# Optimization experiments

Hardware: AMD Instinct MI355X
Metric: run time of the kernel (lower is better)

The kernel has to match this reference:

```python
import jax, jax.numpy as jnp
import numpy as np

EPS = 1e-12
B, C, H, M, E, P = 2, 20000, 64, 8, 200000, 3


def setup_inputs() -> dict:
    key = jax.random.key(0)
    ks = jax.random.split(key, 24)
    inp = {}
    inp["features"] = jax.random.normal(ks[0], (B, C, H), jnp.float32)
    inp["positions"] = jax.random.normal(ks[1], (B, C, P), jnp.float32)
    inp["edge_index"] = jax.random.randint(ks[2], (2, E), 0, C)
    inp["degree"] = jax.random.randint(ks[3], (C,), 1, 33).astype(jnp.float32)
    inp["cell_node_indices"] = jax.random.randint(ks[4], (C, M), 0, C)
    mask = (jax.random.uniform(ks[5], (C, M)) > 0.3).astype(jnp.float32)
    inp["cell_node_mask"] = mask.at[:, 0].set(1.0)  # first node always valid (pad semantics)

    def lin(k, fan_in, fan_out):
        return (jax.random.normal(k, (fan_in, fan_out), jnp.float32) / np.sqrt(fan_in)).astype(jnp.float32)

    # message MLP: Linear(2H+4 -> H), SiLU, Linear(H -> H)
    inp["W1"] = lin(ks[6], 2 * H + 4, H); inp["b1"] = jnp.zeros((H,), jnp.float32)
    inp["W2"] = lin(ks[7], H, H);         inp["b2"] = jnp.zeros((H,), jnp.float32)
    # position MLP: Linear(H -> H), SiLU, Linear(H -> 1)
    inp["P1"] = lin(ks[8], H, H);  inp["pb1"] = jnp.zeros((H,), jnp.float32)
    inp["P2"] = lin(ks[9], H, 1);  inp["pb2"] = jnp.zeros((1,), jnp.float32)
    # update MLP: Linear(2H -> H), SiLU, Linear(H -> H)
    inp["U1"] = lin(ks[10], 2 * H, H); inp["ub1"] = jnp.zeros((H,), jnp.float32)
    inp["U2"] = lin(ks[11], H, H);     inp["ub2"] = jnp.zeros((H,), jnp.float32)
    return inp


def _mlp(x, Wa, ba, Wb, bb):
    return jax.nn.silu(x @ Wa + ba) @ Wb + bb


def _forward(features, positions, edge_index, degree, cell_node_indices, cell_node_mask,
             W1, b1, W2, b2, P1, pb1, P2, pb2, U1, ub1, U2, ub2):
    src, dst = edge_index[0], edge_index[1]
    # gather padded node positions per cell: [B, C, M, P]
    node_pos = positions[:, cell_node_indices]

    h_src = features[:, src]                      # [B,E,H]
    h_dst = features[:, dst]
    rel = positions[:, src] - positions[:, dst]   # [B,E,P]
    dist = jnp.linalg.norm(rel, axis=-1, keepdims=True)  # [B,E,1]

    sp = node_pos[:, src]                         # [B,E,M,P]
    dp = node_pos[:, dst]
    mx = cell_node_mask[src]                      # [E,M]
    my = cell_node_mask[dst]

    # pairwise distances [B,E,M,M] via gram trick (avoids [B,E,M,M,P] intermediate)
    sp2 = jnp.sum(sp * sp, -1)                    # [B,E,M]
    dp2 = jnp.sum(dp * dp, -1)
    cross = jnp.einsum('bemp,benp->bemn', sp, dp)
    d = jnp.sqrt(jnp.maximum(sp2[..., :, None] + dp2[..., None, :] - 2.0 * cross, 0.0) + EPS)

    # masked pairwise-distance sum
    w = mx[:, :, None] * my[:, None, :]           # [E,M,M]
    pairwise = jnp.sum(d * w[None], axis=(-1, -2))  # [B,E]

    # centroid distance
    denx = jnp.maximum(mx.sum(-1, keepdims=True), EPS)  # [E,1]
    deny = jnp.maximum(my.sum(-1, keepdims=True), EPS)
    cx = jnp.sum(sp * mx[None, :, :, None], axis=2) / denx[None]  # [B,E,P]
    cy = jnp.sum(dp * my[None, :, :, None], axis=2) / deny[None]
    centroid = jnp.linalg.norm(cx - cy, axis=-1)  # [B,E]

    # Hausdorff distance (masked min/max)
    inf = jnp.float32(jnp.inf)
    d_xy = jnp.where(my[None, :, None, :] <= 0, inf, d)
    min_xy = jnp.where(mx[None] <= 0, 0.0, d_xy.min(-1))  # [B,E,M]
    h_xy = min_xy.max(-1)                                  # [B,E]
    d_yx = jnp.where(mx[None, :, None, :] <= 0, inf, jnp.swapaxes(d, -1, -2))
    min_yx = jnp.where(my[None] <= 0, 0.0, d_yx.min(-1))
    h_yx = min_yx.max(-1)
    haus = jnp.maximum(h_xy, h_yx)

    invariants = jnp.concatenate([dist, pairwise[..., None], centroid[..., None], haus[..., None]], -1)  # [B,E,4]
    msg_in = jnp.concatenate([h_src, h_dst, invariants], -1)  # [B,E,2H+4]
    messages = _mlp(msg_in, W1, b1, W2, b2)                   # [B,E,H]

    # scatter-aggregate into destination cells, degree-normalize
    agg = jnp.zeros_like(features).at[:, dst].add(messages)
    agg = agg / jnp.maximum(degree, 1.0)[None, :, None]

    # position update
    wts = jnp.tanh(_mlp(messages, P1, pb1, P2, pb2))          # [B,E,1]
    pos_upd = jnp.zeros_like(positions).at[:, dst].add(wts * rel)

    new_features = features + _mlp(jnp.concatenate([features, agg], -1), U1, ub1, U2, ub2)
    new_positions = positions + pos_upd
    return new_features, new_positions


def reference(features, positions, edge_index, degree, cell_node_indices, cell_node_mask,
              W1, b1, W2, b2, P1, pb1, P2, pb2, U1, ub1, U2, ub2):
    return _forward(features, positions, edge_index, degree, cell_node_indices, cell_node_mask,
                    W1, b1, W2, b2, P1, pb1, P2, pb2, U1, ub1, U2, ub2)
```

## Files before the change

kernel.cpp:

```cpp
#include <hip/hip_runtime.h>
#include <hip/hip_bf16.h>

#define B_ 2
#define C_ 20000
#define H_ 64
#define M_ 8
#define E_ 200000
#define P_ 3
#define EPS_ 1e-12f
#define ET_ (E_ / 64)

typedef __attribute__((ext_vector_type(8))) short short8;
typedef __attribute__((ext_vector_type(4))) float float4v;

__device__ __forceinline__ float silu_(float x) {
    return x / (1.f + __expf(-x));
}
__device__ __forceinline__ unsigned short f2b(float f) {
    unsigned u = __float_as_uint(f);
    unsigned r = (u + 0x7FFF + ((u >> 16) & 1)) >> 16;
    return (unsigned short)r;
}
__device__ __forceinline__ float b2f(unsigned short h) {
    return __uint_as_float(((unsigned)h) << 16);
}
__device__ __forceinline__ unsigned pk2u(float a, float b) {
    __hip_bfloat162 h = __float22bfloat162_rn(make_float2(a, b));
    unsigned u; __builtin_memcpy(&u, &h, sizeof(u)); return u;
}

#define W1S_OFF 0
#define W2S_OFF 8192
#define P1S_OFF 12288
#define U1S_OFF 16384
#define U2S_OFF 24576
#define WBUF_ELEMS 28672

#define NB_PREP  120
#define NB_FEATB 2500
#define NB_DESC  157
#define NB_HIST  782
#define NB_COMBO (NB_PREP + NB_FEATB + NB_DESC + NB_HIST)

__global__ __launch_bounds__(256) void combo_kernel(
    const float* __restrict__ W1, const float* __restrict__ W2,
    const float* __restrict__ P1, const float* __restrict__ U1,
    const float* __restrict__ U2, unsigned short* __restrict__ wbuf,
    const float* __restrict__ feat, unsigned short* __restrict__ featb,
    const float* __restrict__ pos, const int* __restrict__ cni,
    const float* __restrict__ mask, float* __restrict__ desc,
    const int* __restrict__ ei, int* __restrict__ cnt)
{
    const int bid = blockIdx.x;
    if (bid < NB_PREP) {
        int t = bid * 256 + threadIdx.x;
        if (t >= WBUF_ELEMS) return;
        const float* W; int e;
        if (t < W2S_OFF)      { W = W1; e = t; }
        else if (t < U1S_OFF) { W = (t < P1S_OFF) ? W2 : P1; e = (t < P1S_OFF) ? t - W2S_OFF : t - P1S_OFF; }
        else if (t < U2S_OFF) { W = U1; e = t - U1S_OFF; }
        else                  { W = U2; e = t - U2S_OFF; }
        int j = e & 7, lane = (e >> 3) & 63, nt = (e >> 9) & 3, kk = e >> 11;
        int k = kk * 32 + ((lane >> 4) * 8) + j;
        int n = nt * 16 + (lane & 15);
        wbuf[t] = f2b(W[k * 64 + n]);
    } else if (bid < NB_PREP + NB_FEATB) {
        int t = (bid - NB_PREP) * 256 + threadIdx.x;
        float4 v = *(const float4*)&feat[(size_t)t * 4];
        *(uint2*)&featb[(size_t)t * 4] = make_uint2(pk2u(v.x, v.y), pk2u(v.z, v.w));
    } else if (bid < NB_PREP + NB_FEATB + NB_DESC) {
        int tid = (bid - NB_PREP - NB_FEATB) * 256 + threadIdx.x;
        if (tid >= B_ * C_) return;
        int b = tid / C_, c = tid - b * C_;
        const float* pb = pos + (size_t)b * C_ * P_;
        float4* D = (float4*)(desc + (size_t)tid * 40);
        int4 n0 = *(const int4*)&cni[c*8];
        int4 n1 = *(const int4*)&cni[c*8 + 4];
        float4 m0 = *(const float4*)&mask[c*8];
        float4 m1 = *(const float4*)&mask[c*8 + 4];
        int ni[8] = {n0.x, n0.y, n0.z, n0.w, n1.x, n1.y, n1.z, n1.w};
        float mm[8] = {m0.x, m0.y, m0.z, m0.w, m1.x, m1.y, m1.z, m1.w};
        float sx = 0.f, sy = 0.f, sz = 0.f, sm = 0.f;
        #pragma unroll
        for (int m = 0; m < 8; ++m) {
            float x = pb[ni[m]*3+0], y = pb[ni[m]*3+1], z = pb[ni[m]*3+2];
            D[m] = make_float4(x, y, z, mm[m]);
            sx += x * mm[m]; sy += y * mm[m]; sz += z * mm[m]; sm += mm[m];
        }
        float inv = 1.f / fmaxf(sm, EPS_);
        D[8] = make_float4(sx * inv, sy * inv, sz * inv, sm);
        D[9] = make_float4(pb[c*3+0], pb[c*3+1], pb[c*3+2], 0.f);
    } else {
        int e = (bid - NB_PREP - NB_FEATB - NB_DESC) * 256 + threadIdx.x;
        if (e >= E_) return;
        atomicAdd(&cnt[ei[E_ + e]], 1);
    }
}

__global__ __launch_bounds__(256) void alloc_kernel(
    const int* __restrict__ cnt, int* __restrict__ cursor, int* __restrict__ total)
{
    int idx = blockIdx.x * 256 + threadIdx.x;
    int lane = threadIdx.x & 63;
    int v = (idx < C_) ? cnt[idx] : 0;
    int inc = v;
    #pragma unroll
    for (int s = 1; s < 64; s <<= 1) {
        int n = __shfl_up(inc, s);
        if (lane >= s) inc += n;
    }
    int wtot = __shfl(inc, 63);
    int base = 0;
    if (lane == 0) base = atomicAdd(total, wtot);
    base = __shfl(base, 0);
    if (idx < C_) cursor[idx] = base + inc - v;
}

__global__ __launch_bounds__(256) void scatter_kernel(
    const int* __restrict__ ei, int* __restrict__ cursor,
    int* __restrict__ ssrc, int* __restrict__ sdst)
{
    int e = blockIdx.x * 256 + threadIdx.x;
    if (e >= E_) return;
    int s = ei[e], d = ei[E_ + e];
    int slot = atomicAdd(&cursor[d], 1);
    ssrc[slot] = s;
    sdst[slot] = d;
}

__global__ __launch_bounds__(256) void edge_kernel(
    const unsigned short* __restrict__ featb,
    const int* __restrict__ ssrc, const int* __restrict__ sdst,
    const float* __restrict__ desc,
    const unsigned short* __restrict__ wbuf, const float* __restrict__ W1,
    const float* __restrict__ b1, const float* __restrict__ b2,
    const float* __restrict__ pb1, const float* __restrict__ P2,
    const float* __restrict__ pb2,
    float* __restrict__ aggf, float* __restrict__ out_pos)
{
    __shared__ unsigned short lds[4 * 3328];

    const int tid  = threadIdx.x;
    const int w    = tid >> 6;
    const int lane = tid & 63;
    const int q    = lane >> 4;
    const int l16  = lane & 15;
    const int w16  = w * 16;

    const int tile = blockIdx.x;
    const int b    = tile / ET_;
    const int i0   = (tile - b * ET_) * 64;
    const int s_l  = ssrc[i0 + lane];
    const int d_l  = sdst[i0 + lane];
    const unsigned short* fb = featb + (size_t)b * C_ * H_;

    unsigned short* Xw = lds + w * 3328;
    unsigned short* Hw = Xw + 2176;
    unsigned short* Mw = Xw;

    const int sg = __shfl(s_l, w16 + l16);
    const int dg = __shfl(d_l, w16 + l16);
    const float4* Ds = (const float4*)(desc + ((size_t)b * C_ + sg) * 40);
    const float4* Dd = (const float4*)(desc + ((size_t)b * C_ + dg) * 40);

    float4 S[8];
    float sp2[8], rowmin[8];
    const float INFV = __builtin_inff();
    #pragma unroll
    for (int i = 0; i < 8; ++i) {
        S[i] = Ds[i];
        sp2[i] = S[i].x*S[i].x + S[i].y*S[i].y + S[i].z*S[i].z;
        rowmin[i] = INFV;
    }
    float pair = 0.f, hyx = 0.f;
    #pragma unroll
    for (int jj = 0; jj < 2; ++jj) {
        float4 Dj = Dd[q*2 + jj];
        float dp2 = Dj.x*Dj.x + Dj.y*Dj.y + Dj.z*Dj.z;
        float colmin = INFV;
        #pragma unroll
        for (int i = 0; i < 8; ++i) {
            float cr = S[i].x*Dj.x + S[i].y*Dj.y + S[i].z*Dj.z;
            float dd = sqrtf(fmaxf(sp2[i] + dp2 - 2.f*cr, 0.f) + EPS_);
            pair += dd * S[i].w * Dj.w;
            rowmin[i] = (Dj.w  > 0.f) ? fminf(rowmin[i], dd) : rowmin[i];
            colmin    = (S[i].w > 0.f) ? fminf(colmin, dd)    : colmin;
        }
        hyx = fmaxf(hyx, (Dj.w > 0.f) ? colmin : 0.f);
    }
    pair += __shfl_xor(pair, 16);  pair += __shfl_xor(pair, 32);
    hyx = fmaxf(hyx, __shfl_xor(hyx, 16));  hyx = fmaxf(hyx, __shfl_xor(hyx, 32));
    #pragma unroll
    for (int i = 0; i < 8; ++i) {
        rowmin[i] = fminf(rowmin[i], __shfl_xor(rowmin[i], 16));
        rowmin[i] = fminf(rowmin[i], __shfl_xor(rowmin[i], 32));
    }
    float hxy = 0.f;
    #pragma unroll
    for (int i = 0; i < 8; ++i)
        hxy = fmaxf(hxy, (S[i].w > 0.f) ? rowmin[i] : 0.f);
    float4 Sc = Ds[8], Dc = Dd[8];
    float cdx = Sc.x - Dc.x, cdy = Sc.y - Dc.y, cdz = Sc.z - Dc.z;
    float4 Sp = Ds[9], Dp = Dd[9];
    const float relx = Sp.x - Dp.x, rely = Sp.y - Dp.y, relz = Sp.z - Dp.z;
    const float ivx = sqrtf(relx*relx + rely*rely + relz*relz);
    const float ivy = pair;
    const float ivz = sqrtf(cdx*cdx + cdy*cdy + cdz*cdz);
    const float ivw = fmaxf(hxy, hyx);

    const int rr4 = lane >> 4, c4 = lane & 15;
    #pragma unroll
    for (int it = 0; it < 4; ++it) {
        int rloc = it * 4 + rr4;
        int r = w16 + rloc;
        int sr = __shfl(s_l, r);
        int dr = __shfl(d_l, r);
        uint2 vs = *(const uint2*)&fb[(size_t)sr * 64 + c4 * 4];
        uint2 vd = *(const uint2*)&fb[(size_t)dr * 64 + c4 * 4];
        *(uint2*)&Xw[rloc*136 + c4*4]      = vs;
        *(uint2*)&Xw[rloc*136 + 64 + c4*4] = vd;
    }

    float4v acc[4];
    #pragma unroll
    for (int nt = 0; nt < 4; ++nt) {
        float bv = b1[nt*16 + l16];
        acc[nt] = (float4v){bv, bv, bv, bv};
    }
    #pragma unroll
    for (int kk = 0; kk < 4; ++kk) {
        short8 a = *(const short8*)&Xw[l16*136 + kk*32 + q*8];
        #pragma unroll
        for (int nt = 0; nt < 4; ++nt) {
            short8 bf = *(const short8*)&wbuf[W1S_OFF + (((kk*4 + nt)*64) + lane) * 8];
            acc[nt] = __builtin_amdgcn_mfma_f32_16x16x32_bf16(a, bf, acc[nt], 0, 0, 0);
        }
    }
    float4 iv[4];
    #pragma unroll
    for (int i = 0; i < 4; ++i) {
        int r = q*4 + i;
        iv[i] = make_float4(__shfl(ivx, r), __shfl(ivy, r),
                            __shfl(ivz, r), __shfl(ivw, r));
    }
    #pragma unroll
    for (int nt = 0; nt < 4; ++nt) {
        float wa = W1[128*64 + nt*16 + l16];
        float wb = W1[129*64 + nt*16 + l16];
        float wc = W1[130*64 + nt*16 + l16];
        float wd = W1[131*64 + nt*16 + l16];
        #pragma unroll
        for (int i = 0; i < 4; ++i)
            acc[nt][i] += iv[i].x*wa + iv[i].y*wb + iv[i].z*wc + iv[i].w*wd;
    }
    #pragma unroll
    for (int nt = 0; nt < 4; ++nt)
        #pragma unroll
        for (int i = 0; i < 4; ++i)
            Hw[(q*4 + i)*72 + nt*16 + l16] = f2b(silu_(acc[nt][i]));

    float4v mac[4];
    #pragma unroll
    for (int nt = 0; nt < 4; ++nt) {
        float bv = b2[nt*16 + l16];
        mac[nt] = (float4v){bv, bv, bv, bv};
    }
    #pragma unroll
    for (int kk = 0; kk < 2; ++kk) {
        short8 a = *(const short8*)&Hw[l16*72 + kk*32 + q*8];
        #pragma unroll
        for (int nt = 0; nt < 4; ++nt) {
            short8 bf = *(const short8*)&wbuf[W2S_OFF + (((kk*4 + nt)*64) + lane) * 8];
            mac[nt] = __builtin_amdgcn_mfma_f32_16x16x32_bf16(a, bf, mac[nt], 0, 0, 0);
        }
    }
    #pragma unroll
    for (int nt = 0; nt < 4; ++nt)
        #pragma unroll
        for (int i = 0; i < 4; ++i)
            Mw[(q*4 + i)*72 + nt*16 + l16] = f2b(mac[nt][i]);

    float4v gac[4];
    #pragma unroll
    for (int nt = 0; nt < 4; ++nt) {
        float bv = pb1[nt*16 + l16];
        gac[nt] = (float4v){bv, bv, bv, bv};
    }
    #pragma unroll
    for (int kk = 0; kk < 2; ++kk) {
        short8 a = *(const short8*)&Mw[l16*72 + kk*32 + q*8];
        #pragma unroll
        for (int nt = 0; nt < 4; ++nt) {
            short8 bf = *(const short8*)&wbuf[P1S_OFF + (((kk*4 + nt)*64) + lane) * 8];
            gac[nt] = __builtin_amdgcn_mfma_f32_16x16x32_bf16(a, bf, gac[nt], 0, 0, 0);
        }
    }
    float p2v[4];
    #pragma unroll
    for (int nt = 0; nt < 4; ++nt) p2v[nt] = P2[nt*16 + l16];
    const float pb2v = pb2[0];

    #pragma unroll
    for (int i = 0; i < 4; ++i) {
        float p = 0.f;
        #pragma unroll
        for (int nt = 0; nt < 4; ++nt) p += silu_(gac[nt][i]) * p2v[nt];
        p += __shfl_xor(p, 8);
        p += __shfl_xor(p, 4);
        p += __shfl_xor(p, 2);
        p += __shfl_xor(p, 1);
        float wt = tanhf(p + pb2v);
        if (l16 == 0) *(float*)&Mw[(q*4 + i)*72 + 64] = wt;
    }

    float mrow[16];
    #pragma unroll
    for (int rr = 0; rr < 16; ++rr) mrow[rr] = b2f(Mw[rr*72 + lane]);
    float wtl = *(const float*)&Mw[l16*72 + 64];

    float* aggB = aggf + (size_t)b * C_ * 64;
    float* opB  = out_pos + (size_t)b * C_ * 3;

    int dprev = __shfl(d_l, w16);
    float colacc = 0.f, pxa = 0.f, pya = 0.f, pza = 0.f;
    #pragma unroll
    for (int rr = 0; rr < 16; ++rr) {
        int dcur = __shfl(d_l, w16 + rr);
        if (dcur != dprev) {
            atomicAdd(&aggB[(size_t)dprev * 64 + lane], colacc);
            if (lane < 3) {
                float v = (lane == 0) ? pxa : (lane == 1) ? pya : pza;
                atomicAdd(&opB[(size_t)dprev * 3 + lane], v);
            }
            colacc = 0.f; pxa = 0.f; pya = 0.f; pza = 0.f;
            dprev = dcur;
        }
        float wt = __shfl(wtl, rr);
        colacc += mrow[rr];
        pxa += wt * __shfl(relx, rr);
        pya += wt * __shfl(rely, rr);
        pza += wt * __shfl(relz, rr);
    }
    atomicAdd(&aggB[(size_t)dprev * 64 + lane], colacc);
    if (lane < 3) {
        float v = (lane == 0) ? pxa : (lane == 1) ? pya : pza;
        atomicAdd(&opB[(size_t)dprev * 3 + lane], v);
    }
}

__global__ __launch_bounds__(256) void node_kernel(
    const float* __restrict__ feat, const unsigned short* __restrict__ featb,
    const float* __restrict__ aggf, const float* __restrict__ deg,
    const unsigned short* __restrict__ wbuf,
    const float* __restrict__ ub1, const float* __restrict__ ub2,
    float* __restrict__ out_feat)
{
    __shared__ unsigned short lds[4 * 3328];

    const int tid  = threadIdx.x;
    const int w    = tid >> 6;
    const int lane = tid & 63;
    const int q    = lane >> 4;
    const int l16  = lane & 15;
    const int g0   = blockIdx.x * 64;

    unsigned short* Xw = lds + w * 3328;
    unsigned short* Hw = Xw + 2176;

    const int rr4 = lane >> 4, c4 = lane & 15;
    #pragma unroll
    for (int it = 0; it < 4; ++it) {
        int rloc = it * 4 + rr4;
        int g = g0 + w*16 + rloc;
        int gc = (g >= C_) ? g - C_ : g;
        float sc = 1.f / fmaxf(deg[gc], 1.f);
        uint2  vf = *(const uint2*)&featb[(size_t)g * 64 + c4 * 4];
        float4 va = *(const float4*)&aggf[(size_t)g * 64 + c4 * 4];
        *(uint2*)&Xw[rloc*136 + c4*4]      = vf;
        *(uint2*)&Xw[rloc*136 + 64 + c4*4] =
            make_uint2(pk2u(va.x*sc, va.y*sc), pk2u(va.z*sc, va.w*sc));
    }

    float4v acc[4];
    #pragma unroll
    for (int nt = 0; nt < 4; ++nt) {
        float bv = ub1[nt*16 + l16];
        acc[nt] = (float4v){bv, bv, bv, bv};
    }
    #pragma unroll
    for (int kk = 0; kk < 4; ++kk) {
        short8 a = *(const short8*)&Xw[l16*136 + kk*32 + q*8];
        #pragma unroll
        for (int nt = 0; nt < 4; ++nt) {
            short8 bf = *(const short8*)&wbuf[U1S_OFF + (((kk*4 + nt)*64) + lane) * 8];
            acc[nt] = __builtin_amdgcn_mfma_f32_16x16x32_bf16(a, bf, acc[nt], 0, 0, 0);
        }
    }
    #pragma unroll
    for (int nt = 0; nt < 4; ++nt)
        #pragma unroll
        for (int i = 0; i < 4; ++i)
            Hw[(q*4 + i)*72 + nt*16 + l16] = f2b(silu_(acc[nt][i]));

    float4v oac[4];
    #pragma unroll
    for (int nt = 0; nt < 4; ++nt) {
        float bv = ub2[nt*16 + l16];
        oac[nt] = (float4v){bv, bv, bv, bv};
    }
    #pragma unroll
    for (int kk = 0; kk < 2; ++kk) {
        short8 a = *(const short8*)&Hw[l16*72 + kk*32 + q*8];
        #pragma unroll
        for (int nt = 0; nt < 4; ++nt) {
            short8 bf = *(const short8*)&wbuf[U2S_OFF + (((kk*4 + nt)*64) + lane) * 8];
            oac[nt] = __builtin_amdgcn_mfma_f32_16x16x32_bf16(a, bf, oac[nt], 0, 0, 0);
        }
    }
    #pragma unroll
    for (int nt = 0; nt < 4; ++nt)
        #pragma unroll
        for (int i = 0; i < 4; ++i) {
            size_t idx = (size_t)(g0 + w*16 + q*4 + i) * 64 + nt*16 + l16;
            out_feat[idx] = feat[idx] + oac[nt][i];
        }
}

extern "C" void kernel_launch(void* const* d_in, const int* in_sizes, int n_in,
                              void* d_out, int out_size, void* d_ws, size_t ws_size,
                              hipStream_t stream) {
    const float* feat = (const float*)d_in[0];
    const float* pos  = (const float*)d_in[1];
    const int*   ei   = (const int*)d_in[2];
    const float* deg  = (const float*)d_in[3];
    const int*   cni  = (const int*)d_in[4];
    const float* mask = (const float*)d_in[5];
    const float* W1   = (const float*)d_in[6];
    const float* b1   = (const float*)d_in[7];
    const float* W2   = (const float*)d_in[8];
    const float* b2   = (const float*)d_in[9];
    const float* P1   = (const float*)d_in[10];
    const float* pb1  = (const float*)d_in[11];
    const float* P2   = (const float*)d_in[12];
    const float* pb2  = (const float*)d_in[13];
    const float* U1   = (const float*)d_in[14];
    const float* ub1  = (const float*)d_in[15];
    const float* U2   = (const float*)d_in[16];
    const float* ub2  = (const float*)d_in[17];

    float* out_feat = (float*)d_out;
    float* out_pos  = out_feat + (size_t)B_ * C_ * H_;

    float* desc = (float*)d_ws;
    float* aggf = desc + (size_t)B_ * C_ * 40;
    unsigned short* featb = (unsigned short*)(aggf + (size_t)B_ * C_ * 64);
    unsigned short* wbuf  = featb + (size_t)B_ * C_ * 64;
    int* cnt    = (int*)(wbuf + WBUF_ELEMS);
    int* total  = cnt + C_;
    int* cursor = total + 1;
    int* ssrc   = cursor + C_;
    int* sdst   = ssrc + E_;

    hipMemsetAsync(cnt, 0, (C_ + 1) * sizeof(int), stream);
    hipMemsetAsync(aggf, 0, (size_t)B_ * C_ * 64 * sizeof(float), stream);
    hipMemcpyAsync(out_pos, pos, (size_t)B_ * C_ * P_ * sizeof(float),
                   hipMemcpyDeviceToDevice, stream);

    combo_kernel<<<NB_COMBO, 256, 0, stream>>>(
        W1, W2, P1, U1, U2, wbuf, feat, featb, pos, cni, mask, desc, ei, cnt);

    alloc_kernel<<<(C_ + 255) / 256, 256, 0, stream>>>(cnt, cursor, total);
    scatter_kernel<<<(E_ + 255) / 256, 256, 0, stream>>>(ei, cursor, ssrc, sdst);

    edge_kernel<<<B_ * ET_, 256, 0, stream>>>(
        featb, ssrc, sdst, desc, wbuf, W1, b1, b2, pb1, P2, pb2, aggf, out_pos);

    node_kernel<<<(B_ * C_) / 64, 256, 0, stream>>>(
        feat, featb, aggf, deg, wbuf, ub1, ub2, out_feat);
}
```

Before: 226.5 us.

## Fold aggregate zeroing and position copy into combo kernel; streamline edge math

Moves the aggf memset and the out_pos device copy into extra blocks of the combo kernel, removing two separate stream operations. The Hausdorff and pairwise distance loop now uses additive infinity masks and a fused per-column sum, which replaces the selects and multiplies. The position scatter is rewritten so that 48 lanes each issue one atomic per edge component, instead of a serial shuffle-accumulate with run-length flushing. Occupancy hints are added to the edge and node kernels. Per-edge position atomics raise the atomic count, and the launch-bound hint may cause register spills.

Result: slower. 252.0 us (+11.2%).

```diff
diff --git a/kernel.cpp b/kernel.cpp
--- a/kernel.cpp
+++ b/kernel.cpp
@@ -36,11 +36,13 @@
 #define U2S_OFF 24576
 #define WBUF_ELEMS 28672
 
-#define NB_PREP  120
-#define NB_FEATB 2500
-#define NB_DESC  157
-#define NB_HIST  782
-#define NB_COMBO (NB_PREP + NB_FEATB + NB_DESC + NB_HIST)
+#define NB_PREP   120
+#define NB_FEATB  2500
+#define NB_DESC   157
+#define NB_HIST   782
+#define NB_AGGZ   2500
+#define NB_PCPY   118
+#define NB_COMBO  (NB_PREP + NB_FEATB + NB_DESC + NB_HIST + NB_AGGZ + NB_PCPY)
 
 __global__ __launch_bounds__(256) void combo_kernel(
     const float* __restrict__ W1, const float* __restrict__ W2,
@@ -49,7 +51,8 @@
     const float* __restrict__ feat, unsigned short* __restrict__ featb,
     const float* __restrict__ pos, const int* __restrict__ cni,
     const float* __restrict__ mask, float* __restrict__ desc,
-    const int* __restrict__ ei, int* __restrict__ cnt)
+    const int* __restrict__ ei, int* __restrict__ cnt,
+    float* __restrict__ aggf, float* __restrict__ out_pos)
 {
     const int bid = blockIdx.x;
     if (bid < NB_PREP) {
@@ -90,10 +93,17 @@
         float inv = 1.f / fmaxf(sm, EPS_);
         D[8] = make_float4(sx * inv, sy * inv, sz * inv, sm);
         D[9] = make_float4(pb[c*3+0], pb[c*3+1], pb[c*3+2], 0.f);
-    } else {
+    } else if (bid < NB_PREP + NB_FEATB + NB_DESC + NB_HIST) {
         int e = (bid - NB_PREP - NB_FEATB - NB_DESC) * 256 + threadIdx.x;
         if (e >= E_) return;
         atomicAdd(&cnt[ei[E_ + e]], 1);
+    } else if (bid < NB_PREP + NB_FEATB + NB_DESC + NB_HIST + NB_AGGZ) {
+        int t = (bid - NB_PREP - NB_FEATB - NB_DESC - NB_HIST) * 256 + threadIdx.x;
+        ((float4*)aggf)[t] = make_float4(0.f, 0.f, 0.f, 0.f);
+    } else {
+        int t = (bid - NB_PREP - NB_FEATB - NB_DESC - NB_HIST - NB_AGGZ) * 256 + threadIdx.x;
+        if (t < (B_ * C_ * P_) / 4)
+            ((float4*)out_pos)[t] = ((const float4*)pos)[t];
     }
 }
 
@@ -128,7 +138,7 @@
     sdst[slot] = d;
 }
 
-__global__ __launch_bounds__(256) void edge_kernel(
+__global__ __launch_bounds__(256, 4) void edge_kernel(
     const unsigned short* __restrict__ featb,
     const int* __restrict__ ssrc, const int* __restrict__ sdst,
     const float* __restrict__ desc,
@@ -163,13 +173,14 @@
     const float4* Ds = (const float4*)(desc + ((size_t)b * C_ + sg) * 40);
     const float4* Dd = (const float4*)(desc + ((size_t)b * C_ + dg) * 40);
 
+    const float INFV = __builtin_inff();
     float4 S[8];
-    float sp2[8], rowmin[8];
-    const float INFV = __builtin_inff();
+    float a_i[8], infm_i[8], rowmin[8];
     #pragma unroll
     for (int i = 0; i < 8; ++i) {
         S[i] = Ds[i];
-        sp2[i] = S[i].x*S[i].x + S[i].y*S[i].y + S[i].z*S[i].z;
+        a_i[i] = S[i].x*S[i].x + S[i].y*S[i].y + S[i].z*S[i].z + EPS_;
+        infm_i[i] = (S[i].w > 0.f) ? 0.f : INFV;
         rowmin[i] = INFV;
     }
     float pair = 0.f, hyx = 0.f;
@@ -177,15 +188,18 @@
     for (int jj = 0; jj < 2; ++jj) {
         float4 Dj = Dd[q*2 + jj];
         float dp2 = Dj.x*Dj.x + Dj.y*Dj.y + Dj.z*Dj.z;
-        float colmin = INFV;
+        float infm_j = (Dj.w > 0.f) ? 0.f : INFV;
+        float colmin = INFV, psum = 0.f;
         #pragma unroll
         for (int i = 0; i < 8; ++i) {
             float cr = S[i].x*Dj.x + S[i].y*Dj.y + S[i].z*Dj.z;
-            float dd = sqrtf(fmaxf(sp2[i] + dp2 - 2.f*cr, 0.f) + EPS_);
-            pair += dd * S[i].w * Dj.w;
-            rowmin[i] = (Dj.w  > 0.f) ? fminf(rowmin[i], dd) : rowmin[i];
-            colmin    = (S[i].w > 0.f) ? fminf(colmin, dd)    : colmin;
-        }
+            float t  = (a_i[i] + dp2) - 2.f*cr;
+            float dd = sqrtf(fmaxf(t, EPS_));
+            psum = fmaf(dd, S[i].w, psum);
+            rowmin[i] = fminf(rowmin[i], dd + infm_j);
+            colmin    = fminf(colmin,    dd + infm_i[i]);
+        }
+        pair = fmaf(Dj.w, psum, pair);
         hyx = fmaxf(hyx, (Dj.w > 0.f) ? colmin : 0.f);
     }
     pair += __shfl_xor(pair, 16);  pair += __shfl_xor(pair, 32);
@@ -313,42 +327,40 @@
         if (l16 == 0) *(float*)&Mw[(q*4 + i)*72 + 64] = wt;
     }
 
-    float mrow[16];
-    #pragma unroll
-    for (int rr = 0; rr < 16; ++rr) mrow[rr] = b2f(Mw[rr*72 + lane]);
-    float wtl = *(const float*)&Mw[l16*72 + 64];
-
     float* aggB = aggf + (size_t)b * C_ * 64;
     float* opB  = out_pos + (size_t)b * C_ * 3;
 
+    float wtl = *(const float*)&Mw[l16*72 + 64];
+    float gx = wtl * relx, gy = wtl * rely, gz = wtl * relz;
+    int e3 = lane / 3;
+    int c3 = lane - e3 * 3;
+    float sx = __shfl(gx, e3);
+    float sy = __shfl(gy, e3);
+    float sz = __shfl(gz, e3);
+    float val = (c3 == 0) ? sx : (c3 == 1) ? sy : sz;
+    int de = __shfl(d_l, w16 + e3);
+    if (lane < 48) atomicAdd(&opB[(size_t)de * 3 + c3], val);
+
+    float mrow[16];
+    #pragma unroll
+    for (int rr = 0; rr < 16; ++rr) mrow[rr] = b2f(Mw[rr*72 + lane]);
+
     int dprev = __shfl(d_l, w16);
-    float colacc = 0.f, pxa = 0.f, pya = 0.f, pza = 0.f;
+    float colacc = 0.f;
     #pragma unroll
     for (int rr = 0; rr < 16; ++rr) {
         int dcur = __shfl(d_l, w16 + rr);
         if (dcur != dprev) {
             atomicAdd(&aggB[(size_t)dprev * 64 + lane], colacc);
-            if (lane < 3) {
-                float v = (lane == 0) ? pxa : (lane == 1) ? pya : pza;
-                atomicAdd(&opB[(size_t)dprev * 3 + lane], v);
-            }
-            colacc = 0.f; pxa = 0.f; pya = 0.f; pza = 0.f;
+            colacc = 0.f;
             dprev = dcur;
         }
-        float wt = __shfl(wtl, rr);
         colacc += mrow[rr];
-        pxa += wt * __shfl(relx, rr);
-        pya += wt * __shfl(rely, rr);
-        pza += wt * __shfl(relz, rr);
     }
     atomicAdd(&aggB[(size_t)dprev * 64 + lane], colacc);
-    if (lane < 3) {
-        float v = (lane == 0) ? pxa : (lane == 1) ? pya : pza;
-        atomicAdd(&opB[(size_t)dprev * 3 + lane], v);
-    }
-}
-
-__global__ __launch_bounds__(256) void node_kernel(
+}
+
+__global__ __launch_bounds__(256, 4) void node_kernel(
     const float* __restrict__ feat, const unsigned short* __restrict__ featb,
     const float* __restrict__ aggf, const float* __restrict__ deg,
     const unsigned short* __restrict__ wbuf,
@@ -462,12 +474,10 @@
     int* sdst   = ssrc + E_;
 
     hipMemsetAsync(cnt, 0, (C_ + 1) * sizeof(int), stream);
-    hipMemsetAsync(aggf, 0, (size_t)B_ * C_ * 64 * sizeof(float), stream);
-    hipMemcpyAsync(out_pos, pos, (size_t)B_ * C_ * P_ * sizeof(float),
-                   hipMemcpyDeviceToDevice, stream);
 
     combo_kernel<<<NB_COMBO, 256, 0, stream>>>(
-        W1, W2, P1, U1, U2, wbuf, feat, featb, pos, cni, mask, desc, ei, cnt);
+        W1, W2, P1, U1, U2, wbuf, feat, featb, pos, cni, mask, desc, ei, cnt,
+        aggf, out_pos);
 
     alloc_kernel<<<(C_ + 255) / 256, 256, 0, stream>>>(cnt, cursor, total);
     scatter_kernel<<<(E_ + 255) / 256, 256, 0, stream>>>(ei, cursor, ssrc, sdst);
```
